# Optimization experiments

Measured on AMD Instinct MI355X. Metric: run time of the kernel, lower is better.

## Reference

```python
import jax, jax.numpy as jnp
import numpy as np

N = 50000
E = 800000
IN_DIM = 128
HID = 256
NCLASS = 40
ORDER = 3
LOCAL_NOISE = 0.5


def setup_inputs() -> dict:
    key = jax.random.key(0)
    ks = jax.random.split(key, 8)
    feats = jax.random.normal(ks[0], (N, IN_DIM), dtype=jnp.float32)
    edge_row = jax.random.randint(ks[1], (E,), 0, N, dtype=jnp.int32)
    edge_col = jax.random.randint(ks[2], (E,), 0, N, dtype=jnp.int32)
    edge_vals = jax.random.uniform(ks[3], (E,), dtype=jnp.float32) / 16.0  # ~row-normalized adjacency
    W1 = jax.random.normal(ks[4], (IN_DIM, HID), dtype=jnp.float32) * (1.0 / np.sqrt(IN_DIM))
    b1 = jnp.zeros((HID,), dtype=jnp.float32)
    W2 = jax.random.normal(ks[5], (HID, NCLASS), dtype=jnp.float32) * (1.0 / np.sqrt(HID))
    b2 = jnp.zeros((NCLASS,), dtype=jnp.float32)
    return {"feats": feats, "edge_row": edge_row, "edge_col": edge_col,
            "edge_vals": edge_vals, "W1": W1, "b1": b1, "W2": W2, "b2": b2}


def _spmm(edge_row, edge_col, edge_vals, x):
    # y[r] = sum_e vals[e] * x[col[e]] for edges with row[e]==r
    msgs = edge_vals[:, None] * x[edge_col]  # [E, D]
    return jax.ops.segment_sum(msgs, edge_row, num_segments=N)


def reference(feats, edge_row, edge_col, edge_vals, W1, b1, W2, b2):
    # eval path: drop_node scales by (1 - drop_rate)
    x = feats * (1.0 - LOCAL_NOISE)
    # GRANDConv_NX: K-hop propagation with running-sum average
    y = x
    h = x
    for _ in range(ORDER):
        h = _spmm(edge_row, edge_col, edge_vals, h)
        y = y + h
    feat = y / (ORDER + 1.0)
    # MLP (use_bn=False, dropout inactive at eval)
    h1 = jax.nn.relu(feat @ W1 + b1)
    logits = h1 @ W2 + b2
    # MLP.forward applies log_softmax, outer forward applies it again
    out = jax.nn.log_softmax(jax.nn.log_softmax(logits, axis=-1), axis=-1)
    return out
```

## Files before the change

### kernel.cpp

```cpp
#include <hip/hip_runtime.h>
#include <math.h>

#define N_NODES 50000
#define N_EDGES 800000
#define IN_DIM 128
#define HID 256
#define NCLASS 40

#define SCAN_NBLK 49

#define HBLK 256
#define EPB  3125
#define PK   12500
#define CS_G 4
#define CS_HPG 64

typedef __attribute__((ext_vector_type(8))) short short8;
typedef __attribute__((ext_vector_type(4))) float floatx4;
typedef __attribute__((ext_vector_type(4))) unsigned uintx4;

__device__ inline unsigned bf16pair(float a, float b) {
    unsigned ua = __float_as_uint(a), ub = __float_as_uint(b);
    ua = (ua + 0x7fffu + ((ua >> 16) & 1u)) >> 16;
    ub = (ub + 0x7fffu + ((ub >> 16) & 1u)) >> 16;
    return ua | (ub << 16);
}
__device__ inline unsigned bf16bits(float a) {
    unsigned ua = __float_as_uint(a);
    return (ua + 0x7fffu + ((ua >> 16) & 1u)) >> 16;
}
__device__ inline float bf_lo(unsigned u) { return __uint_as_float(u << 16); }
__device__ inline float bf_hi(unsigned u) { return __uint_as_float(u & 0xffff0000u); }

__global__ void prep_kernel(const float4* __restrict__ f4,
                            uint2* __restrict__ fb16,
                            const float* __restrict__ W1,
                            uint4* __restrict__ W1frag,
                            const float* __restrict__ W2,
                            uint4* __restrict__ W2frag) {
    int i = blockIdx.x * blockDim.x + threadIdx.x;
    float4 v = f4[i];
    fb16[i] = make_uint2(bf16pair(v.x, v.y), bf16pair(v.z, v.w));
    if (i < 4096) {
        int f = i;
        int h = f >> 11, rem = f & 2047;
        int t = rem >> 8, s = (rem >> 6) & 3, l = rem & 63;
        int q = l >> 4, n16 = l & 15;
        int n = h * 128 + t * 16 + n16;
        int kb = s * 32 + q * 8;
        unsigned p[4];
        #pragma unroll
        for (int jj = 0; jj < 4; ++jj) {
            float a = W1[(size_t)(kb + 2 * jj) * HID + n];
            float b = W1[(size_t)(kb + 2 * jj + 1) * HID + n];
            p[jj] = bf16pair(a, b);
        }
        W1frag[f] = make_uint4(p[0], p[1], p[2], p[3]);
    } else if (i < 4096 + 1536) {
        int f2 = i - 4096;
        int nt = f2 >> 9;
        int rem = f2 & 511;
        int ks = rem >> 6, l = rem & 63;
        int col = nt * 16 + (l & 15);
        int k = ks * 32 + (l >> 4) * 8;
        unsigned p[4];
        #pragma unroll
        for (int jj = 0; jj < 4; ++jj) {
            float a = (col < NCLASS) ? W2[(size_t)(k + 2 * jj) * NCLASS + col] : 0.f;
            float b = (col < NCLASS) ? W2[(size_t)(k + 2 * jj + 1) * NCLASS + col] : 0.f;
            p[jj] = bf16pair(a, b);
        }
        W2frag[f2] = make_uint4(p[0], p[1], p[2], p[3]);
    }
}

__global__ __launch_bounds__(1024) void hist_kernel(const int* __restrict__ rows,
                                                    unsigned* __restrict__ hist) {
    __shared__ unsigned h[PK];
    int t = threadIdx.x;
    for (int i = t; i < PK / 4; i += 1024)
        ((uint4*)h)[i] = make_uint4(0u, 0u, 0u, 0u);
    __syncthreads();
    int e0 = blockIdx.x * EPB;
    for (int i = t; i < EPB; i += 1024) {
        int r = rows[e0 + i];
        atomicAdd(&h[r >> 2], 1u << ((r & 3) * 8));
    }
    __syncthreads();
    unsigned* out = hist + (size_t)blockIdx.x * PK;
    for (int i = t; i < PK / 4; i += 1024)
        ((uint4*)out)[i] = ((const uint4*)h)[i];
}

__global__ __launch_bounds__(1024) void colscan_kernel(const unsigned* __restrict__ hist,
                                                       unsigned* __restrict__ base,
                                                       unsigned* __restrict__ goff,
                                                       int* __restrict__ counts,
                                                       int* __restrict__ blockSums) {
    __shared__ unsigned lsum[CS_G][256];
    int tid = threadIdx.x;
    int g = tid >> 8;
    int c = tid & 255;
    int colq = blockIdx.x * 256 + c;
    unsigned run = 0;
    if (colq < PK) {
        #pragma unroll 8
        for (int i = 0; i < CS_HPG; ++i) {
            int b = g * CS_HPG + i;
            unsigned v = hist[(size_t)b * PK + colq];
            base[(size_t)b * PK + colq] = run;
            run += v;
        }
    }
    lsum[g][c] = run;
    __syncthreads();
    unsigned off = 0;
    #pragma unroll
    for (int gg = 0; gg < CS_G; ++gg) {
        unsigned v = lsum[gg][c];
        if (gg < g) off += v;
    }
    unsigned tot = off + run;
    if (colq < PK) {
        goff[(size_t)g * PK + colq] = off;
        if (g == CS_G - 1)
            *(int4*)(counts + 4 * colq) = make_int4((int)(tot & 0xffu), (int)((tot >> 8) & 0xffu),
                                                    (int)((tot >> 16) & 0xffu), (int)(tot >> 24));
    }
    int s = 0;
    if (g == CS_G - 1 && colq < PK)
        s = (int)((tot & 0xffu) + ((tot >> 8) & 0xffu) + ((tot >> 16) & 0xffu) + (tot >> 24));
    #pragma unroll
    for (int o = 32; o >= 1; o >>= 1)
        s += __shfl_xor(s, o);
    __shared__ int wsum[16];
    int lane = tid & 63, wid = tid >> 6;
    if (lane == 0) wsum[wid] = s;
    __syncthreads();
    if (tid == 0) {
        int acc = 0;
        #pragma unroll
        for (int i = 0; i < 16; ++i) acc += wsum[i];
        blockSums[blockIdx.x] = acc;
    }
}

__global__ __launch_bounds__(256) void local_scan_kernel(const int* __restrict__ counts,
                                                         const int* __restrict__ blockSums,
                                                         int* __restrict__ row_start) {
    __shared__ int wsum[4];
    __shared__ int boff;
    int t = threadIdx.x;
    if (t < 64) {
        int x = (t < SCAN_NBLK) ? blockSums[t] : 0;
        #pragma unroll
        for (int off = 1; off < 64; off <<= 1) {
            int y = __shfl_up(x, off);
            if (t >= off) x += y;
        }
        int excl = __shfl_up(x, 1);
        if (t == 0) excl = 0;
        if (t == blockIdx.x) boff = excl;
        if (blockIdx.x == SCAN_NBLK - 1 && t == SCAN_NBLK - 1)
            row_start[N_NODES] = x;
    }
    int base = blockIdx.x * 1024 + t * 4;
    int4 c = make_int4(0, 0, 0, 0);
    if (base < N_NODES) c = *(const int4*)(counts + base);
    int s0 = c.x, s1 = s0 + c.y, s2 = s1 + c.z, s3 = s2 + c.w;
    int tsum = s3;
    int lane = t & 63, wid = t >> 6;
    int x = tsum;
    #pragma unroll
    for (int off = 1; off < 64; off <<= 1) {
        int y = __shfl_up(x, off);
        if (lane >= off) x += y;
    }
    if (lane == 63) wsum[wid] = x;
    __syncthreads();
    int woff = 0;
    for (int i = 0; i < 4; ++i)
        if (i < wid) woff += wsum[i];
    int excl = x - tsum + woff + boff;
    if (base < N_NODES) {
        int4 rs = make_int4(excl, excl + s0, excl + s1, excl + s2);
        *(int4*)(row_start + base) = rs;
    }
}

__global__ __launch_bounds__(1024) void scatter2_kernel(const int* __restrict__ rows,
                                                        const int* __restrict__ cols,
                                                        const float* __restrict__ vals,
                                                        const unsigned* __restrict__ base,
                                                        const unsigned* __restrict__ goff,
                                                        const int* __restrict__ row_start,
                                                        unsigned* __restrict__ csr_cv) {
    __shared__ unsigned cur[PK];
    int t = threadIdx.x;
    const uint4* bb = (const uint4*)(base + (size_t)blockIdx.x * PK);
    const uint4* gg = (const uint4*)(goff + (size_t)(blockIdx.x >> 6) * PK);
    for (int i = t; i < PK / 4; i += 1024) {
        uint4 b = bb[i], o = gg[i];
        ((uint4*)cur)[i] = make_uint4(b.x + o.x, b.y + o.y, b.z + o.z, b.w + o.w);
    }
    __syncthreads();
    int e0 = blockIdx.x * EPB;
    for (int i = t; i < EPB; i += 1024) {
        int e = e0 + i;
        int r = rows[e];
        unsigned sh = (unsigned)(r & 3) * 8u;
        unsigned old = atomicAdd(&cur[r >> 2], 1u << sh);
        int pos = row_start[r] + (int)((old >> sh) & 0xffu);
        csr_cv[pos] = ((unsigned)cols[e] << 16) | bf16bits(vals[e]);
    }
}

template <int MODE>
__global__ void spmm_csr(const int* __restrict__ row_start,
                         const unsigned* __restrict__ csr_cv,
                         const uintx4* __restrict__ Hin4,
                         uintx4* __restrict__ Hout4,
                         const float* __restrict__ feats,
                         const uintx4* __restrict__ h1b4,
                         const uintx4* __restrict__ h2b4) {
    int wave = (blockIdx.x * blockDim.x + threadIdx.x) >> 6;
    int lane = threadIdx.x & 63;
    if (wave >= N_NODES) return;
    int p = lane >> 4;
    int q = lane & 15;
    int start = row_start[wave];
    int end   = row_start[wave + 1];
    float acc[8] = {};
    for (int base = start; base < end; base += 64) {
        int idx = base + lane;
        unsigned u = 0;
        if (idx < end) u = __builtin_nontemporal_load(csr_cv + idx);
        int cnt = min(64, end - base);
        for (int j = 0; j < cnt; j += 16) {
            unsigned uj0 = __shfl(u, j + p);
            unsigned uj1 = __shfl(u, j + 4 + p);
            unsigned uj2 = __shfl(u, j + 8 + p);
            unsigned uj3 = __shfl(u, j + 12 + p);
            int c0 = uj0 >> 16, c1 = uj1 >> 16, c2 = uj2 >> 16, c3 = uj3 >> 16;
            float v0 = __uint_as_float(uj0 << 16);
            float v1 = __uint_as_float(uj1 << 16);
            float v2 = __uint_as_float(uj2 << 16);
            float v3 = __uint_as_float(uj3 << 16);
            uintx4 h0 = Hin4[(size_t)c0 * 16 + q];
            uintx4 h1 = Hin4[(size_t)c1 * 16 + q];
            uintx4 h2 = Hin4[(size_t)c2 * 16 + q];
            uintx4 h3 = Hin4[(size_t)c3 * 16 + q];
            acc[0] += v0 * bf_lo(h0.x); acc[1] += v0 * bf_hi(h0.x);
            acc[2] += v0 * bf_lo(h0.y); acc[3] += v0 * bf_hi(h0.y);
            acc[4] += v0 * bf_lo(h0.z); acc[5] += v0 * bf_hi(h0.z);
            acc[6] += v0 * bf_lo(h0.w); acc[7] += v0 * bf_hi(h0.w);
            acc[0] += v1 * bf_lo(h1.x); acc[1] += v1 * bf_hi(h1.x);
            acc[2] += v1 * bf_lo(h1.y); acc[3] += v1 * bf_hi(h1.y);
            acc[4] += v1 * bf_lo(h1.z); acc[5] += v1 * bf_hi(h1.z);
            acc[6] += v1 * bf_lo(h1.w); acc[7] += v1 * bf_hi(h1.w);
            acc[0] += v2 * bf_lo(h2.x); acc[1] += v2 * bf_hi(h2.x);
            acc[2] += v2 * bf_lo(h2.y); acc[3] += v2 * bf_hi(h2.y);
            acc[4] += v2 * bf_lo(h2.z); acc[5] += v2 * bf_hi(h2.z);
            acc[6] += v2 * bf_lo(h2.w); acc[7] += v2 * bf_hi(h2.w);
            acc[0] += v3 * bf_lo(h3.x); acc[1] += v3 * bf_hi(h3.x);
            acc[2] += v3 * bf_lo(h3.y); acc[3] += v3 * bf_hi(h3.y);
            acc[4] += v3 * bf_lo(h3.z); acc[5] += v3 * bf_hi(h3.z);
            acc[6] += v3 * bf_lo(h3.w); acc[7] += v3 * bf_hi(h3.w);
        }
    }
    #pragma unroll
    for (int i = 0; i < 8; ++i) {
        acc[i] += __shfl_xor(acc[i], 16);
        acc[i] += __shfl_xor(acc[i], 32);
    }
    if (p == 0) {
        size_t o16 = (size_t)wave * 16 + q;
        if (MODE == 1) {
            #pragma unroll
            for (int i = 0; i < 8; ++i) acc[i] *= 0.5f;
        } else if (MODE == 2) {
            size_t of = (size_t)wave * IN_DIM + q * 8;
            floatx4 f0 = __builtin_nontemporal_load((const floatx4*)(feats + of));
            floatx4 f1 = __builtin_nontemporal_load((const floatx4*)(feats + of + 4));
            uintx4 a = __builtin_nontemporal_load(h1b4 + o16);
            uintx4 b = __builtin_nontemporal_load(h2b4 + o16);
            acc[0] += 0.5f * f0.x + bf_lo(a.x) + bf_lo(b.x);
            acc[1] += 0.5f * f0.y + bf_hi(a.x) + bf_hi(b.x);
            acc[2] += 0.5f * f0.z + bf_lo(a.y) + bf_lo(b.y);
            acc[3] += 0.5f * f0.w + bf_hi(a.y) + bf_hi(b.y);
            acc[4] += 0.5f * f1.x + bf_lo(a.z) + bf_lo(b.z);
            acc[5] += 0.5f * f1.y + bf_hi(a.z) + bf_hi(b.z);
            acc[6] += 0.5f * f1.z + bf_lo(a.w) + bf_lo(b.w);
            acc[7] += 0.5f * f1.w + bf_hi(a.w) + bf_hi(b.w);
        }
        uintx4 rv;
        rv.x = bf16pair(acc[0], acc[1]);
        rv.y = bf16pair(acc[2], acc[3]);
        rv.z = bf16pair(acc[4], acc[5]);
        rv.w = bf16pair(acc[6], acc[7]);
        __builtin_nontemporal_store(rv, Hout4 + o16);
    }
}

#define H1_STRIDE 264
__global__ __launch_bounds__(256) void mlp_fused(const uint4* __restrict__ yb4,
                                                 const uint4* __restrict__ W1frag,
                                                 const uint4* __restrict__ W2frag,
                                                 const float* __restrict__ bias1,
                                                 const float* __restrict__ b2,
                                                 float* __restrict__ Out) {
    __shared__ unsigned short h1u[64 * H1_STRIDE];
    int tid = threadIdx.x;
    int w = tid >> 6, lane = tid & 63;
    int q = lane >> 4, c16 = lane & 15;
    int row0 = blockIdx.x * 64;
    int arow = row0 + w * 16 + c16;

    union { uint4 u; short8 v; } au[4], bu, af;
    if (arow < N_NODES) {
        #pragma unroll
        for (int s = 0; s < 4; ++s)
            au[s].u = yb4[(size_t)arow * 16 + 4 * s + q];
    } else {
        #pragma unroll
        for (int s = 0; s < 4; ++s)
            au[s].u = make_uint4(0u, 0u, 0u, 0u);
    }

    #pragma unroll 4
    for (int ct = 0; ct < 16; ++ct) {
        floatx4 acc = {0.f, 0.f, 0.f, 0.f};
        #pragma unroll
        for (int s = 0; s < 4; ++s) {
            bu.u = W1frag[(ct * 4 + s) * 64 + lane];
            acc = __builtin_amdgcn_mfma_f32_16x16x32_bf16(au[s].v, bu.v, acc, 0, 0, 0);
        }
        int col = ct * 16 + c16;
        float bs = bias1[col];
        #pragma unroll
        for (int r = 0; r < 4; ++r) {
            float v = 0.25f * acc[r] + bs;
            v = v > 0.f ? v : 0.f;
            h1u[(w * 16 + q * 4 + r) * H1_STRIDE + col] = (unsigned short)bf16bits(v);
        }
    }
    __syncthreads();

    floatx4 acc2[3] = {{0.f,0.f,0.f,0.f},{0.f,0.f,0.f,0.f},{0.f,0.f,0.f,0.f}};
    const unsigned* h1w = (const unsigned*)h1u;
    #pragma unroll
    for (int ks = 0; ks < 8; ++ks) {
        af.u = *(const uint4*)&h1w[(w * 16 + c16) * (H1_STRIDE / 2) + ks * 16 + q * 4];
        #pragma unroll
        for (int nt = 0; nt < 3; ++nt) {
            bu.u = W2frag[nt * 512 + ks * 64 + lane];
            acc2[nt] = __builtin_amdgcn_mfma_f32_16x16x32_bf16(af.v, bu.v, acc2[nt], 0, 0, 0);
        }
    }

    float bb[3];
    #pragma unroll
    for (int nt = 0; nt < 3; ++nt) {
        int col = nt * 16 + c16;
        bb[nt] = (col < NCLASS) ? b2[col] : 0.f;
    }
    #pragma unroll
    for (int r = 0; r < 4; ++r) {
        int gr = row0 + w * 16 + q * 4 + r;
        float z[3];
        #pragma unroll
        for (int nt = 0; nt < 3; ++nt) z[nt] = acc2[nt][r] + bb[nt];
        if (c16 >= 8) z[2] = -INFINITY;
        float m = fmaxf(fmaxf(z[0], z[1]), z[2]);
        #pragma unroll
        for (int off = 1; off < 16; off <<= 1) m = fmaxf(m, __shfl_xor(m, off));
        float s = expf(z[0] - m) + expf(z[1] - m) + ((c16 < 8) ? expf(z[2] - m) : 0.f);
        #pragma unroll
        for (int off = 1; off < 16; off <<= 1) s += __shfl_xor(s, off);
        float l1 = m + logf(s);
        #pragma unroll
        for (int nt = 0; nt < 3; ++nt) z[nt] -= l1;
        float m2 = fmaxf(fmaxf(z[0], z[1]), z[2]);
        #pragma unroll
        for (int off = 1; off < 16; off <<= 1) m2 = fmaxf(m2, __shfl_xor(m2, off));
        float s2 = expf(z[0] - m2) + expf(z[1] - m2) + ((c16 < 8) ? expf(z[2] - m2) : 0.f);
        #pragma unroll
        for (int off = 1; off < 16; off <<= 1) s2 += __shfl_xor(s2, off);
        float l2 = m2 + logf(s2);
        if (gr < N_NODES) {
            #pragma unroll
            for (int nt = 0; nt < 3; ++nt) {
                int col = nt * 16 + c16;
                if (col < NCLASS)
                    Out[(size_t)gr * NCLASS + col] = z[nt] - l2;
            }
        }
    }
}

extern "C" void kernel_launch(void* const* d_in, const int* in_sizes, int n_in,
                              void* d_out, int out_size, void* d_ws, size_t ws_size,
                              hipStream_t stream) {
    const float* feats   = (const float*)d_in[0];
    const int*   e_row   = (const int*)d_in[1];
    const int*   e_col   = (const int*)d_in[2];
    const float* e_vals  = (const float*)d_in[3];
    const float* W1      = (const float*)d_in[4];
    const float* b1      = (const float*)d_in[5];
    const float* W2      = (const float*)d_in[6];
    const float* b2      = (const float*)d_in[7];
    float* out = (float*)d_out;

    float* ws    = (float*)d_ws;
    uint4* ybf4  = (uint4*)ws;
    unsigned* hist = (unsigned*)ws;
    uint4* W1frag = (uint4*)(ws + (size_t)N_NODES * IN_DIM / 2);
    uint4* W2frag = (uint4*)(ws + 3250000);
    int*   counts = (int*)(ws + 3300000);
    unsigned* goff = (unsigned*)(ws + 3400000);
    uint4* fb16_4 = (uint4*)(ws + (size_t)N_NODES * IN_DIM);
    uint4* h1b4  = (uint4*)(ws + (size_t)N_NODES * IN_DIM * 3 / 2);
    uint4* h2b4  = (uint4*)(ws + (size_t)N_NODES * IN_DIM * 2);
    unsigned* basep = (unsigned*)(ws + (size_t)N_NODES * IN_DIM * 5 / 2);

    unsigned* csr_cv = (unsigned*)d_out;
    int*   row_start = (int*)d_out + 2 * N_EDGES;
    int*   blockSums = row_start + N_NODES + 4;

    const int ELEMS4 = N_NODES * IN_DIM / 4;
    prep_kernel<<<ELEMS4 / 256, 256, 0, stream>>>((const float4*)feats, (uint2*)fb16_4,
                                                  W1, W1frag, W2, W2frag);

    hist_kernel<<<HBLK, 1024, 0, stream>>>(e_row, hist);
    colscan_kernel<<<SCAN_NBLK, 1024, 0, stream>>>(hist, basep, goff, counts, blockSums);
    local_scan_kernel<<<SCAN_NBLK, 256, 0, stream>>>(counts, blockSums, row_start);
    scatter2_kernel<<<HBLK, 1024, 0, stream>>>(e_row, e_col, e_vals, basep, goff,
                                               row_start, csr_cv);

    const int SPMM_BLOCKS = N_NODES / 4;
    spmm_csr<1><<<SPMM_BLOCKS, 256, 0, stream>>>(row_start, csr_cv, (const uintx4*)fb16_4,
                                                 (uintx4*)h1b4, nullptr, nullptr, nullptr);
    spmm_csr<0><<<SPMM_BLOCKS, 256, 0, stream>>>(row_start, csr_cv, (const uintx4*)h1b4,
                                                 (uintx4*)h2b4, nullptr, nullptr, nullptr);
    spmm_csr<2><<<SPMM_BLOCKS, 256, 0, stream>>>(row_start, csr_cv, (const uintx4*)h2b4,
                                                 (uintx4*)ybf4, feats,
                                                 (const uintx4*)h1b4, (const uintx4*)h2b4);

    mlp_fused<<<(N_NODES + 63) / 64, 256, 0, stream>>>(ybf4, W1frag, W2frag, b1, b2, out);
}
```

Baseline: 229.1 us.

## Process two rows per wave in SpMM and fuse prep with histogram kernel

```diff
diff --git a/kernel.cpp b/kernel.cpp
--- a/kernel.cpp
+++ b/kernel.cpp
@@ -32,21 +32,41 @@
 __device__ inline float bf_lo(unsigned u) { return __uint_as_float(u << 16); }
 __device__ inline float bf_hi(unsigned u) { return __uint_as_float(u & 0xffff0000u); }
 
-__global__ void prep_kernel(const float4* __restrict__ f4,
-                            uint2* __restrict__ fb16,
-                            const float* __restrict__ W1,
-                            uint4* __restrict__ W1frag,
-                            const float* __restrict__ W2,
-                            uint4* __restrict__ W2frag) {
-    int i = blockIdx.x * blockDim.x + threadIdx.x;
-    float4 v = f4[i];
-    fb16[i] = make_uint2(bf16pair(v.x, v.y), bf16pair(v.z, v.w));
-    if (i < 4096) {
-        int f = i;
-        int h = f >> 11, rem = f & 2047;
-        int t = rem >> 8, s = (rem >> 6) & 3, l = rem & 63;
+#define FMA8(A, v, h) do { \
+    A[0] += (v) * bf_lo((h).x); A[1] += (v) * bf_hi((h).x); \
+    A[2] += (v) * bf_lo((h).y); A[3] += (v) * bf_hi((h).y); \
+    A[4] += (v) * bf_lo((h).z); A[5] += (v) * bf_hi((h).z); \
+    A[6] += (v) * bf_lo((h).w); A[7] += (v) * bf_hi((h).w); } while (0)
+
+__global__ __launch_bounds__(1024) void prep_hist_kernel(const float4* __restrict__ f4,
+                                                         uint2* __restrict__ fb16,
+                                                         const float* __restrict__ W1,
+                                                         uint4* __restrict__ W1frag,
+                                                         const float* __restrict__ W2,
+                                                         uint4* __restrict__ W2frag,
+                                                         const int* __restrict__ rows,
+                                                         unsigned* __restrict__ hist) {
+    __shared__ unsigned h[PK];
+    int t = threadIdx.x;
+    for (int i = t; i < PK / 4; i += 1024)
+        ((uint4*)h)[i] = make_uint4(0u, 0u, 0u, 0u);
+    __syncthreads();
+    int e0 = blockIdx.x * EPB;
+    for (int i = t; i < EPB; i += 1024) {
+        int r = rows[e0 + i];
+        atomicAdd(&h[r >> 2], 1u << ((r & 3) * 8));
+    }
+    int gid = blockIdx.x * 1024 + t;
+    for (int i = gid; i < N_NODES * IN_DIM / 4; i += HBLK * 1024) {
+        float4 v = f4[i];
+        fb16[i] = make_uint2(bf16pair(v.x, v.y), bf16pair(v.z, v.w));
+    }
+    if (gid < 4096) {
+        int f = gid;
+        int hh = f >> 11, rem = f & 2047;
+        int tt = rem >> 8, s = (rem >> 6) & 3, l = rem & 63;
         int q = l >> 4, n16 = l & 15;
-        int n = h * 128 + t * 16 + n16;
+        int n = hh * 128 + tt * 16 + n16;
         int kb = s * 32 + q * 8;
         unsigned p[4];
         #pragma unroll
@@ -56,8 +76,8 @@
             p[jj] = bf16pair(a, b);
         }
         W1frag[f] = make_uint4(p[0], p[1], p[2], p[3]);
-    } else if (i < 4096 + 1536) {
-        int f2 = i - 4096;
+    } else if (gid < 4096 + 1536) {
+        int f2 = gid - 4096;
         int nt = f2 >> 9;
         int rem = f2 & 511;
         int ks = rem >> 6, l = rem & 63;
@@ -71,20 +91,6 @@
             p[jj] = bf16pair(a, b);
         }
         W2frag[f2] = make_uint4(p[0], p[1], p[2], p[3]);
-    }
-}
-
-__global__ __launch_bounds__(1024) void hist_kernel(const int* __restrict__ rows,
-                                                    unsigned* __restrict__ hist) {
-    __shared__ unsigned h[PK];
-    int t = threadIdx.x;
-    for (int i = t; i < PK / 4; i += 1024)
-        ((uint4*)h)[i] = make_uint4(0u, 0u, 0u, 0u);
-    __syncthreads();
-    int e0 = blockIdx.x * EPB;
-    for (int i = t; i < EPB; i += 1024) {
-        int r = rows[e0 + i];
-        atomicAdd(&h[r >> 2], 1u << ((r & 3) * 8));
     }
     __syncthreads();
     unsigned* out = hist + (size_t)blockIdx.x * PK;
@@ -216,89 +222,110 @@
 }
 
 template <int MODE>
-__global__ void spmm_csr(const int* __restrict__ row_start,
-                         const unsigned* __restrict__ csr_cv,
-                         const uintx4* __restrict__ Hin4,
-                         uintx4* __restrict__ Hout4,
-                         const float* __restrict__ feats,
-                         const uintx4* __restrict__ h1b4,
-                         const uintx4* __restrict__ h2b4) {
-    int wave = (blockIdx.x * blockDim.x + threadIdx.x) >> 6;
+__device__ inline void spmm_store(int row, float* acc, int q,
+                                  uintx4* __restrict__ Hout4,
+                                  const float* __restrict__ feats,
+                                  const uintx4* __restrict__ h1b4,
+                                  const uintx4* __restrict__ h2b4) {
+    size_t o16 = (size_t)row * 16 + q;
+    if (MODE == 1) {
+        #pragma unroll
+        for (int i = 0; i < 8; ++i) acc[i] *= 0.5f;
+    } else if (MODE == 2) {
+        size_t of = (size_t)row * IN_DIM + q * 8;
+        floatx4 f0 = __builtin_nontemporal_load((const floatx4*)(feats + of));
+        floatx4 f1 = __builtin_nontemporal_load((const floatx4*)(feats + of + 4));
+        uintx4 a = __builtin_nontemporal_load(h1b4 + o16);
+        uintx4 b = __builtin_nontemporal_load(h2b4 + o16);
+        acc[0] += 0.5f * f0.x + bf_lo(a.x) + bf_lo(b.x);
+        acc[1] += 0.5f * f0.y + bf_hi(a.x) + bf_hi(b.x);
+        acc[2] += 0.5f * f0.z + bf_lo(a.y) + bf_lo(b.y);
+        acc[3] += 0.5f * f0.w + bf_hi(a.y) + bf_hi(b.y);
+        acc[4] += 0.5f * f1.x + bf_lo(a.z) + bf_lo(b.z);
+        acc[5] += 0.5f * f1.y + bf_hi(a.z) + bf_hi(b.z);
+        acc[6] += 0.5f * f1.z + bf_lo(a.w) + bf_lo(b.w);
+        acc[7] += 0.5f * f1.w + bf_hi(a.w) + bf_hi(b.w);
+    }
+    uintx4 rv;
+    rv.x = bf16pair(acc[0], acc[1]);
+    rv.y = bf16pair(acc[2], acc[3]);
+    rv.z = bf16pair(acc[4], acc[5]);
+    rv.w = bf16pair(acc[6], acc[7]);
+    __builtin_nontemporal_store(rv, Hout4 + o16);
+}
+
+template <int MODE>
+__global__ __launch_bounds__(256) void spmm_csr(const int* __restrict__ row_start,
+                                                const unsigned* __restrict__ csr_cv,
+                                                const uintx4* __restrict__ Hin4,
+                                                uintx4* __restrict__ Hout4,
+                                                const float* __restrict__ feats,
+                                                const uintx4* __restrict__ h1b4,
+                                                const uintx4* __restrict__ h2b4) {
+    int wv = (blockIdx.x * blockDim.x + threadIdx.x) >> 6;
     int lane = threadIdx.x & 63;
-    if (wave >= N_NODES) return;
+    int pr = wv * 2;
     int p = lane >> 4;
     int q = lane & 15;
-    int start = row_start[wave];
-    int end   = row_start[wave + 1];
-    float acc[8] = {};
-    for (int base = start; base < end; base += 64) {
-        int idx = base + lane;
-        unsigned u = 0;
-        if (idx < end) u = __builtin_nontemporal_load(csr_cv + idx);
-        int cnt = min(64, end - base);
-        for (int j = 0; j < cnt; j += 16) {
-            unsigned uj0 = __shfl(u, j + p);
-            unsigned uj1 = __shfl(u, j + 4 + p);
-            unsigned uj2 = __shfl(u, j + 8 + p);
-            unsigned uj3 = __shfl(u, j + 12 + p);
-            int c0 = uj0 >> 16, c1 = uj1 >> 16, c2 = uj2 >> 16, c3 = uj3 >> 16;
-            float v0 = __uint_as_float(uj0 << 16);
-            float v1 = __uint_as_float(uj1 << 16);
-            float v2 = __uint_as_float(uj2 << 16);
-            float v3 = __uint_as_float(uj3 << 16);
-            uintx4 h0 = Hin4[(size_t)c0 * 16 + q];
-            uintx4 h1 = Hin4[(size_t)c1 * 16 + q];
-            uintx4 h2 = Hin4[(size_t)c2 * 16 + q];
-            uintx4 h3 = Hin4[(size_t)c3 * 16 + q];
-            acc[0] += v0 * bf_lo(h0.x); acc[1] += v0 * bf_hi(h0.x);
-            acc[2] += v0 * bf_lo(h0.y); acc[3] += v0 * bf_hi(h0.y);
-            acc[4] += v0 * bf_lo(h0.z); acc[5] += v0 * bf_hi(h0.z);
-            acc[6] += v0 * bf_lo(h0.w); acc[7] += v0 * bf_hi(h0.w);
-            acc[0] += v1 * bf_lo(h1.x); acc[1] += v1 * bf_hi(h1.x);
-            acc[2] += v1 * bf_lo(h1.y); acc[3] += v1 * bf_hi(h1.y);
-            acc[4] += v1 * bf_lo(h1.z); acc[5] += v1 * bf_hi(h1.z);
-            acc[6] += v1 * bf_lo(h1.w); acc[7] += v1 * bf_hi(h1.w);
-            acc[0] += v2 * bf_lo(h2.x); acc[1] += v2 * bf_hi(h2.x);
-            acc[2] += v2 * bf_lo(h2.y); acc[3] += v2 * bf_hi(h2.y);
-            acc[4] += v2 * bf_lo(h2.z); acc[5] += v2 * bf_hi(h2.z);
-            acc[6] += v2 * bf_lo(h2.w); acc[7] += v2 * bf_hi(h2.w);
-            acc[0] += v3 * bf_lo(h3.x); acc[1] += v3 * bf_hi(h3.x);
-            acc[2] += v3 * bf_lo(h3.y); acc[3] += v3 * bf_hi(h3.y);
-            acc[4] += v3 * bf_lo(h3.z); acc[5] += v3 * bf_hi(h3.z);
-            acc[6] += v3 * bf_lo(h3.w); acc[7] += v3 * bf_hi(h3.w);
-        }
+    int s0 = row_start[pr];
+    int e0 = row_start[pr + 1];
+    int e1 = row_start[pr + 2];
+    float a0[8] = {}, a1[8] = {};
+    int b0 = s0, b1 = e0;
+    while (b0 < e0 || b1 < e1) {
+        unsigned u0 = 0, u1 = 0;
+        if (b0 + lane < e0) u0 = __builtin_nontemporal_load(csr_cv + b0 + lane);
+        if (b1 + lane < e1) u1 = __builtin_nontemporal_load(csr_cv + b1 + lane);
+        int m0 = e0 - b0, m1 = e1 - b1;
+        int m = m0 > m1 ? m0 : m1;
+        if (m > 64) m = 64;
+        for (int j = 0; j < m; j += 16) {
+            unsigned x0 = __shfl(u0, j + p);
+            unsigned x1 = __shfl(u0, j + 4 + p);
+            unsigned x2 = __shfl(u0, j + 8 + p);
+            unsigned x3 = __shfl(u0, j + 12 + p);
+            unsigned y0 = __shfl(u1, j + p);
+            unsigned y1 = __shfl(u1, j + 4 + p);
+            unsigned y2 = __shfl(u1, j + 8 + p);
+            unsigned y3 = __shfl(u1, j + 12 + p);
+            uintx4 hx0 = Hin4[(size_t)(x0 >> 16) * 16 + q];
+            uintx4 hx1 = Hin4[(size_t)(x1 >> 16) * 16 + q];
+            uintx4 hx2 = Hin4[(size_t)(x2 >> 16) * 16 + q];
+            uintx4 hx3 = Hin4[(size_t)(x3 >> 16) * 16 + q];
+            uintx4 hy0 = Hin4[(size_t)(y0 >> 16) * 16 + q];
+            uintx4 hy1 = Hin4[(size_t)(y1 >> 16) * 16 + q];
+            uintx4 hy2 = Hin4[(size_t)(y2 >> 16) * 16 + q];
+            uintx4 hy3 = Hin4[(size_t)(y3 >> 16) * 16 + q];
+            float vx0 = __uint_as_float(x0 << 16);
+            float vx1 = __uint_as_float(x1 << 16);
+            float vx2 = __uint_as_float(x2 << 16);
+            float vx3 = __uint_as_float(x3 << 16);
+            float vy0 = __uint_as_float(y0 << 16);
+            float vy1 = __uint_as_float(y1 << 16);
+            float vy2 = __uint_as_float(y2 << 16);
+            float vy3 = __uint_as_float(y3 << 16);
+            FMA8(a0, vx0, hx0);
+            FMA8(a0, vx1, hx1);
+            FMA8(a0, vx2, hx2);
+            FMA8(a0, vx3, hx3);
+            FMA8(a1, vy0, hy0);
+            FMA8(a1, vy1, hy1);
+            FMA8(a1, vy2, hy2);
+            FMA8(a1, vy3, hy3);
+        }
+        b0 += 64;
+        b1 += 64;
     }
     #pragma unroll
     for (int i = 0; i < 8; ++i) {
-        acc[i] += __shfl_xor(acc[i], 16);
-        acc[i] += __shfl_xor(acc[i], 32);
+        a0[i] += __shfl_xor(a0[i], 16);
+        a0[i] += __shfl_xor(a0[i], 32);
+        a1[i] += __shfl_xor(a1[i], 16);
+        a1[i] += __shfl_xor(a1[i], 32);
     }
     if (p == 0) {
-        size_t o16 = (size_t)wave * 16 + q;
-        if (MODE == 1) {
-            #pragma unroll
-            for (int i = 0; i < 8; ++i) acc[i] *= 0.5f;
-        } else if (MODE == 2) {
-            size_t of = (size_t)wave * IN_DIM + q * 8;
-            floatx4 f0 = __builtin_nontemporal_load((const floatx4*)(feats + of));
-            floatx4 f1 = __builtin_nontemporal_load((const floatx4*)(feats + of + 4));
-            uintx4 a = __builtin_nontemporal_load(h1b4 + o16);
-            uintx4 b = __builtin_nontemporal_load(h2b4 + o16);
-            acc[0] += 0.5f * f0.x + bf_lo(a.x) + bf_lo(b.x);
-            acc[1] += 0.5f * f0.y + bf_hi(a.x) + bf_hi(b.x);
-            acc[2] += 0.5f * f0.z + bf_lo(a.y) + bf_lo(b.y);
-            acc[3] += 0.5f * f0.w + bf_hi(a.y) + bf_hi(b.y);
-            acc[4] += 0.5f * f1.x + bf_lo(a.z) + bf_lo(b.z);
-            acc[5] += 0.5f * f1.y + bf_hi(a.z) + bf_hi(b.z);
-            acc[6] += 0.5f * f1.z + bf_lo(a.w) + bf_lo(b.w);
-            acc[7] += 0.5f * f1.w + bf_hi(a.w) + bf_hi(b.w);
-        }
-        uintx4 rv;
-        rv.x = bf16pair(acc[0], acc[1]);
-        rv.y = bf16pair(acc[2], acc[3]);
-        rv.z = bf16pair(acc[4], acc[5]);
-        rv.w = bf16pair(acc[6], acc[7]);
-        __builtin_nontemporal_store(rv, Hout4 + o16);
+        spmm_store<MODE>(pr,     a0, q, Hout4, feats, h1b4, h2b4);
+        spmm_store<MODE>(pr + 1, a1, q, Hout4, feats, h1b4, h2b4);
     }
 }
 
@@ -344,7 +371,6 @@
             h1u[(w * 16 + q * 4 + r) * H1_STRIDE + col] = (unsigned short)bf16bits(v);
         }
     }
-    __syncthreads();
 
     floatx4 acc2[3] = {{0.f,0.f,0.f,0.f},{0.f,0.f,0.f,0.f},{0.f,0.f,0.f,0.f}};
     const unsigned* h1w = (const unsigned*)h1u;
@@ -427,17 +453,15 @@
     int*   row_start = (int*)d_out + 2 * N_EDGES;
     int*   blockSums = row_start + N_NODES + 4;
 
-    const int ELEMS4 = N_NODES * IN_DIM / 4;
-    prep_kernel<<<ELEMS4 / 256, 256, 0, stream>>>((const float4*)feats, (uint2*)fb16_4,
-                                                  W1, W1frag, W2, W2frag);
-
-    hist_kernel<<<HBLK, 1024, 0, stream>>>(e_row, hist);
+    prep_hist_kernel<<<HBLK, 1024, 0, stream>>>((const float4*)feats, (uint2*)fb16_4,
+                                                W1, W1frag, W2, W2frag, e_row, hist);
+
     colscan_kernel<<<SCAN_NBLK, 1024, 0, stream>>>(hist, basep, goff, counts, blockSums);
     local_scan_kernel<<<SCAN_NBLK, 256, 0, stream>>>(counts, blockSums, row_start);
     scatter2_kernel<<<HBLK, 1024, 0, stream>>>(e_row, e_col, e_vals, basep, goff,
                                                row_start, csr_cv);
 
-    const int SPMM_BLOCKS = N_NODES / 4;
+    const int SPMM_BLOCKS = N_NODES / 8;
     spmm_csr<1><<<SPMM_BLOCKS, 256, 0, stream>>>(row_start, csr_cv, (const uintx4*)fb16_4,
                                                  (uintx4*)h1b4, nullptr, nullptr, nullptr);
     spmm_csr<0><<<SPMM_BLOCKS, 256, 0, stream>>>(row_start, csr_cv, (const uintx4*)h1b4,
```

New measurement: 237.5 us. 3.7% more time.
